# Kernel tuning notes

Hardware: AMD Instinct MI355X
Metric: run time of the kernel (lower is better)

The kernel has to match this reference:

```python
import jax, jax.numpy as jnp
import numpy as np

NUM_HEADS = 8


def setup_inputs() -> dict:
    key = jax.random.key(0)
    ks = jax.random.split(key, 16)
    B, Ct, Co, H, W = 1, 256, 128, 64, 64
    s = lambda k, *shape: jax.random.normal(k, shape, dtype=jnp.float32) * 0.02
    return {
        "thermal_features": jax.random.normal(ks[0], (B, Ct, H, W), dtype=jnp.float32),
        "optical_features": jax.random.normal(ks[1], (B, Co, H, W), dtype=jnp.float32),
        "emissivity_map": jax.random.uniform(ks[2], (B, 1, H, W), dtype=jnp.float32),
        "Wq": s(ks[3], Ct, Ct), "bq": jnp.zeros((Ct,), jnp.float32),
        "Wk": s(ks[4], Ct, Co), "bk": jnp.zeros((Ct,), jnp.float32),
        "Wv": s(ks[5], Ct, Co), "bv": jnp.zeros((Ct,), jnp.float32),
        "conv1_w": s(ks[6], 32, 1, 3, 3), "conv1_b": jnp.zeros((32,), jnp.float32),
        "conv2_w": s(ks[7], NUM_HEADS, 32, 1, 1), "conv2_b": jnp.zeros((NUM_HEADS,), jnp.float32),
        "Wp": s(ks[8], Ct, Ct), "bp": jnp.zeros((Ct,), jnp.float32),
    }


def reference(thermal_features, optical_features, emissivity_map,
              Wq, bq, Wk, bk, Wv, bv, conv1_w, conv1_b, conv2_w, conv2_b, Wp, bp):
    B, Ct, H, W = thermal_features.shape
    Co = optical_features.shape[1]
    N = H * W
    h = NUM_HEADS
    d = Ct // h
    scale = d ** (-0.5)

    # flatten spatial -> tokens: [B, N, C]
    t_flat = thermal_features.reshape(B, Ct, N).transpose(0, 2, 1)
    o_flat = optical_features.reshape(B, Co, N).transpose(0, 2, 1)

    # projections, split heads: [B, h, N, d]
    q = (t_flat @ Wq.T + bq).reshape(B, N, h, d).transpose(0, 2, 1, 3)
    k = (o_flat @ Wk.T + bk).reshape(B, N, h, d).transpose(0, 2, 1, 3)
    v = (o_flat @ Wv.T + bv).reshape(B, N, h, d).transpose(0, 2, 1, 3)

    # full attention scores: [B, h, N, N]
    attn = jnp.einsum('bhqd,bhkd->bhqk', q, k) * scale

    # emissivity gate: Conv(1->32, 3x3, pad 1) -> ReLU -> Conv(32->h, 1x1) -> Sigmoid
    g = jax.lax.conv_general_dilated(emissivity_map, conv1_w, (1, 1), 'SAME',
                                     dimension_numbers=('NCHW', 'OIHW', 'NCHW'))
    g = jax.nn.relu(g + conv1_b[None, :, None, None])
    g = jax.lax.conv_general_dilated(g, conv2_w, (1, 1), 'SAME',
                                     dimension_numbers=('NCHW', 'OIHW', 'NCHW'))
    g = jax.nn.sigmoid(g + conv2_b[None, :, None, None])  # [B, h, H, W]
    g = g.reshape(B, h, N)[..., None]  # [B, h, N, 1] gates query rows

    attn = jax.nn.softmax(attn * g, axis=-1)  # dropout is identity in eval

    out = jnp.einsum('bhqk,bhkd->bhqd', attn, v)  # [B, h, N, d]
    out = out.transpose(0, 2, 1, 3).reshape(B, N, Ct)
    out = out @ Wp.T + bp
    return out.transpose(0, 2, 1).reshape(B, Ct, H, W)
```

## Files before the change

kernel.cpp:

```cpp
#include <hip/hip_runtime.h>
#include <hip/hip_bf16.h>

#define N_TOK 4096
#define CT 256

typedef __attribute__((ext_vector_type(8))) short bf16x8;
typedef __attribute__((ext_vector_type(16))) float f32x16;

__device__ __forceinline__ unsigned pkbf(float a, float b) {
  float2 t; t.x = a; t.y = b;
  __hip_bfloat162 h = __float22bfloat162_rn(t);
  return *reinterpret_cast<unsigned*>(&h);
}

#if __has_builtin(__builtin_amdgcn_exp2f)
__device__ __forceinline__ float fexp2(float x) { return __builtin_amdgcn_exp2f(x); }
#else
__device__ __forceinline__ float fexp2(float x) { return exp2f(x); }
#endif

__global__ __launch_bounds__(256) void prep_kernel(
    const float* __restrict__ thermal, const float* __restrict__ optical,
    const float* __restrict__ Wq, const float* __restrict__ Wk,
    const float* __restrict__ Wv, const float* __restrict__ Wp,
    const float* __restrict__ em, const float* __restrict__ w1,
    const float* __restrict__ b1, const float* __restrict__ w2,
    const float* __restrict__ b2,
    unsigned short* __restrict__ Xbt, unsigned short* __restrict__ Xbo,
    unsigned short* __restrict__ Wall, float* __restrict__ g)
{
  __shared__ unsigned short tile[64][264];
  const int bx = blockIdx.x, tid = threadIdx.x;
  if (bx < 128) {
    const bool th = (bx < 64);
    const float* X = th ? thermal : optical;
    unsigned short* Xb = th ? Xbt : Xbo;
    const int CIN = th ? 256 : 128;
    const int n0 = (th ? bx : bx - 64) * 64;
    const int nl = tid & 63;
    const int cw = (tid >> 6) * 4;
    for (int c0 = 0; c0 < CIN; c0 += 16) {
      int c = c0 + cw;
      float x0 = X[(size_t)(c + 0) * N_TOK + n0 + nl];
      float x1 = X[(size_t)(c + 1) * N_TOK + n0 + nl];
      float x2 = X[(size_t)(c + 2) * N_TOK + n0 + nl];
      float x3 = X[(size_t)(c + 3) * N_TOK + n0 + nl];
      uint2 w; w.x = pkbf(x0, x1); w.y = pkbf(x2, x3);
      *(uint2*)&tile[nl][c] = w;
    }
    __syncthreads();
    const int n = tid >> 2, q = tid & 3;
    const int cb = q * (CIN / 4);
    for (int j = 0; j < CIN / 4; j += 4)
      *(uint2*)(Xb + (size_t)(n0 + n) * CIN + cb + j) = *(const uint2*)&tile[n][cb + j];
  } else if (bx < 224) {
    int i = (bx - 128) * 2048 + tid * 8;
    const float* src; int off;
    if (i < 65536)       { src = Wq; off = 0; }
    else if (i < 98304)  { src = Wk; off = 65536; }
    else if (i < 131072) { src = Wv; off = 98304; }
    else                 { src = Wp; off = 131072; }
    float4 f0 = *(const float4*)(src + (i - off));
    float4 f1 = *(const float4*)(src + (i - off) + 4);
    uint4 o;
    o.x = pkbf(f0.x, f0.y); o.y = pkbf(f0.z, f0.w);
    o.z = pkbf(f1.x, f1.y); o.w = pkbf(f1.z, f1.w);
    *(uint4*)(Wall + i) = o;
  } else {
    int n = (bx - 224) * 256 + tid;
    int y = n >> 6, x = n & 63;
    float e[9];
#pragma unroll
    for (int dy = 0; dy < 3; dy++)
#pragma unroll
      for (int dx = 0; dx < 3; dx++) {
        int yy = y + dy - 1, xx = x + dx - 1;
        e[dy * 3 + dx] = (yy >= 0 && yy < 64 && xx >= 0 && xx < 64)
                             ? em[yy * 64 + xx] : 0.f;
      }
    float c1[32];
#pragma unroll
    for (int oc = 0; oc < 32; oc++) {
      float a = b1[oc];
#pragma unroll
      for (int t = 0; t < 9; t++) a = fmaf(e[t], w1[oc * 9 + t], a);
      c1[oc] = fmaxf(a, 0.f);
    }
#pragma unroll
    for (int hh = 0; hh < 8; hh++) {
      float a = b2[hh];
#pragma unroll
      for (int oc = 0; oc < 32; oc++) a = fmaf(c1[oc], w2[hh * 32 + oc], a);
      g[hh * N_TOK + n] = 1.f / (1.f + __expf(-a));
    }
  }
}

template <int CIN>
__device__ __forceinline__ void gemm_tile(
    const unsigned short* __restrict__ xp, const unsigned short* __restrict__ wp,
    f32x16& accE, f32x16& accO)
{
#pragma unroll
  for (int c = 0; c < CIN; c += 32) {
    bf16x8 a0 = *(const bf16x8*)(xp + c);
    bf16x8 b0 = *(const bf16x8*)(wp + c);
    bf16x8 a1 = *(const bf16x8*)(xp + c + 16);
    bf16x8 b1 = *(const bf16x8*)(wp + c + 16);
    accE = __builtin_amdgcn_mfma_f32_32x32x16_bf16(a0, b0, accE, 0, 0, 0);
    accO = __builtin_amdgcn_mfma_f32_32x32x16_bf16(a1, b1, accO, 0, 0, 0);
  }
}

__global__ __launch_bounds__(256) void qkv_kernel(
    const unsigned short* __restrict__ Xbt, const unsigned short* __restrict__ Xbo,
    const unsigned short* __restrict__ Wall,
    const float* __restrict__ bq, const float* __restrict__ bk,
    const float* __restrict__ bv, const float* __restrict__ g,
    unsigned short* __restrict__ Qh, unsigned short* __restrict__ Kh,
    unsigned short* __restrict__ Vf)
{
  __shared__ float ldsT[4][32][33];
  const int tid = threadIdx.x;
  const int wave = tid >> 6, lane = tid & 63;
  const int l31 = lane & 31, hi = lane >> 5;
  const int y = blockIdx.y;
  const int head = y & 7;
  const int n0 = blockIdx.x * 128 + wave * 32;

  f32x16 accE, accO;
#pragma unroll
  for (int i = 0; i < 16; i++) { accE[i] = 0.f; accO[i] = 0.f; }
  float bo;
  if (y < 8) {
    gemm_tile<256>(Xbt + (size_t)(n0 + l31) * 256 + hi * 8,
                   Wall + (size_t)(head * 32 + l31) * 256 + hi * 8, accE, accO);
    bo = bq[head * 32 + l31];
  } else if (y < 16) {
    gemm_tile<128>(Xbo + (size_t)(n0 + l31) * 128 + hi * 8,
                   Wall + 65536 + (size_t)(head * 32 + l31) * 128 + hi * 8, accE, accO);
    bo = bk[head * 32 + l31];
  } else {
    gemm_tile<128>(Xbo + (size_t)(n0 + l31) * 128 + hi * 8,
                   Wall + 98304 + (size_t)(head * 32 + l31) * 128 + hi * 8, accE, accO);
    bo = bv[head * 32 + l31];
  }
  float val[16];
#pragma unroll
  for (int r = 0; r < 16; r++) val[r] = accE[r] + accO[r] + bo;

  if (y < 8) {
    const float QSC = 0.17677669529663689f * 1.4426950408889634f;
#pragma unroll
    for (int r = 0; r < 16; r++) {
      int t = n0 + (r & 3) + 8 * (r >> 2) + 4 * hi;
      val[r] *= QSC * g[head * N_TOK + t];
    }
  }

#pragma unroll
  for (int r = 0; r < 16; r++)
    ldsT[wave][(r & 3) + 8 * (r >> 2) + 4 * hi][l31] = val[r];

  if (y < 16) {
    unsigned pk[8];
#pragma unroll
    for (int i = 0; i < 8; i++)
      pk[i] = pkbf(ldsT[wave][l31][16 * hi + 2 * i],
                   ldsT[wave][l31][16 * hi + 2 * i + 1]);
    unsigned short* dst = (y < 8 ? Qh : Kh) +
        ((size_t)head * N_TOK + n0 + l31) * 32 + 16 * hi;
    *(uint4*)dst = make_uint4(pk[0], pk[1], pk[2], pk[3]);
    *(uint4*)(dst + 8) = make_uint4(pk[4], pk[5], pk[6], pk[7]);
  } else {
    unsigned pk[8];
#pragma unroll
    for (int i = 0; i < 8; i++)
      pk[i] = pkbf(ldsT[wave][16 * hi + 2 * i][l31],
                   ldsT[wave][16 * hi + 2 * i + 1][l31]);
    unsigned short* dst = Vf +
        (((size_t)head * 256 + (n0 >> 4) + hi) * 32 + l31) * 16;
    *(uint4*)dst = make_uint4(pk[0], pk[1], pk[2], pk[3]);
    *(uint4*)(dst + 8) = make_uint4(pk[4], pk[5], pk[6], pk[7]);
  }
}

__global__ __launch_bounds__(256, 4) void attn_kernel(
    const unsigned short* __restrict__ Qh, const unsigned short* __restrict__ Kh,
    const unsigned short* __restrict__ Vf,
    unsigned short* __restrict__ Ob, float* __restrict__ ls, int kps)
{
  __shared__ float ldsT[4][32][33];
  const int tid = threadIdx.x;
  const int wave = tid >> 6, lane = tid & 63;
  const int l31 = lane & 31, hi = lane >> 5;
  const int hh = blockIdx.x >> 5;
  const int qb = blockIdx.x & 31;
  const int split = blockIdx.y;
  const int qrow0 = qb * 128 + wave * 32;
  const int kbase0 = split * kps;

  const unsigned short* qrow = Qh + ((size_t)hh * N_TOK + qrow0 + l31) * 32;
  const bf16x8 qf0 = *(const bf16x8*)(qrow + hi * 8);
  const bf16x8 qf1 = *(const bf16x8*)(qrow + 16 + hi * 8);

  const unsigned short* kb_base = Kh + (size_t)hh * (N_TOK * 32);
  const unsigned short* vf_base = Vf + (size_t)hh * (256 * 32 * 16);

  f32x16 acc, zero16;
#pragma unroll
  for (int i = 0; i < 16; i++) { acc[i] = 0.f; zero16[i] = 0.f; }
  float lsum = 0.f;

#define LK(kb, s) (*(const bf16x8*)(kb_base + (size_t)((kb) + l31) * 32 + (s) * 16 + hi * 8))
#define LV(kt2)   (*(const bf16x8*)(vf_base + (size_t)((kt2) * 32 + l31) * 16 + hi * 8))

  bf16x8 kf0 = LK(kbase0, 0), kf1 = LK(kbase0, 1);
  bf16x8 vb0 = LV(kbase0 >> 4), vb1 = LV((kbase0 >> 4) + 1);

#pragma unroll 2
  for (int kt = 0; kt < kps; kt += 32) {
    const int nxt = (kt + 32 < kps) ? (kbase0 + kt + 32) : kbase0;
    bf16x8 nk0 = LK(nxt, 0), nk1 = LK(nxt, 1);
    bf16x8 nv0 = LV(nxt >> 4), nv1 = LV((nxt >> 4) + 1);

    f32x16 s = __builtin_amdgcn_mfma_f32_32x32x16_bf16(kf0, qf0, zero16, 0, 0, 0);
    s = __builtin_amdgcn_mfma_f32_32x32x16_bf16(kf1, qf1, s, 0, 0, 0);

    float p[16];
#pragma unroll
    for (int r = 0; r < 16; r++) p[r] = fexp2(s[r]);

    lsum += (((p[0] + p[1]) + (p[2] + p[3])) + ((p[4] + p[5]) + (p[6] + p[7]))) +
            (((p[8] + p[9]) + (p[10] + p[11])) + ((p[12] + p[13]) + (p[14] + p[15])));

    unsigned a0 = pkbf(p[0], p[1]),   a1 = pkbf(p[2], p[3]);
    unsigned b0 = pkbf(p[4], p[5]),   b1 = pkbf(p[6], p[7]);
    unsigned c0 = pkbf(p[8], p[9]),   c1 = pkbf(p[10], p[11]);
    unsigned d0 = pkbf(p[12], p[13]), d1 = pkbf(p[14], p[15]);
    asm("v_permlane32_swap_b32 %0, %1" : "+v"(a0), "+v"(b0));
    asm("v_permlane32_swap_b32 %0, %1" : "+v"(a1), "+v"(b1));
    asm("v_permlane32_swap_b32 %0, %1" : "+v"(c0), "+v"(d0));
    asm("v_permlane32_swap_b32 %0, %1" : "+v"(c1), "+v"(d1));
    union { unsigned w[4]; bf16x8 v; } u0, u1;
    u0.w[0] = a0; u0.w[1] = a1; u0.w[2] = b0; u0.w[3] = b1;
    u1.w[0] = c0; u1.w[1] = c1; u1.w[2] = d0; u1.w[3] = d1;

    acc = __builtin_amdgcn_mfma_f32_32x32x16_bf16(u0.v, vb0, acc, 0, 0, 0);
    acc = __builtin_amdgcn_mfma_f32_32x32x16_bf16(u1.v, vb1, acc, 0, 0, 0);

    kf0 = nk0; kf1 = nk1; vb0 = nv0; vb1 = nv1;
  }
#undef LK
#undef LV

  float lt = lsum + __shfl_xor(lsum, 32);
  if (hi == 0)
    ls[((size_t)split * 8 + hh) * N_TOK + qrow0 + l31] = lt;

#pragma unroll
  for (int r = 0; r < 16; r++)
    ldsT[wave][(r & 3) + 8 * (r >> 2) + 4 * hi][l31] = acc[r];
  unsigned pk[8];
#pragma unroll
  for (int i = 0; i < 8; i++)
    pk[i] = pkbf(ldsT[wave][l31][16 * hi + 2 * i],
                 ldsT[wave][l31][16 * hi + 2 * i + 1]);
  unsigned short* dst =
      Ob + (((size_t)split * 8 + hh) * N_TOK + qrow0 + l31) * 32 + 16 * hi;
  *(uint4*)dst = make_uint4(pk[0], pk[1], pk[2], pk[3]);
  *(uint4*)(dst + 8) = make_uint4(pk[4], pk[5], pk[6], pk[7]);
}

__global__ __launch_bounds__(256) void reduce_kernel(
    const unsigned short* __restrict__ Ob, const float* __restrict__ ls,
    unsigned short* __restrict__ Ab, int ksplit)
{
  int gid = blockIdx.x * 256 + threadIdx.x;
  int n = gid >> 5, c8 = (gid & 31) * 8;
  int hh = c8 >> 5, cc = c8 & 31;
  float o[8];
#pragma unroll
  for (int i = 0; i < 8; i++) o[i] = 0.f;
  float l = 0.f;
  for (int s = 0; s < ksplit; s++) {
    uint4 raw = *(const uint4*)(Ob + (((size_t)s * 8 + hh) * N_TOK + n) * 32 + cc);
    unsigned w[4] = {raw.x, raw.y, raw.z, raw.w};
#pragma unroll
    for (int i = 0; i < 4; i++) {
      o[2 * i]     += __uint_as_float(w[i] << 16);
      o[2 * i + 1] += __uint_as_float(w[i] & 0xffff0000u);
    }
    l += ls[((size_t)s * 8 + hh) * N_TOK + n];
  }
  float inv = 1.f / l;
  unsigned pk[4];
#pragma unroll
  for (int i = 0; i < 4; i++)
    pk[i] = pkbf(o[2 * i] * inv, o[2 * i + 1] * inv);
  *(uint4*)(Ab + (size_t)n * CT + c8) = make_uint4(pk[0], pk[1], pk[2], pk[3]);
}

__global__ __launch_bounds__(256) void pout_kernel(
    const unsigned short* __restrict__ Ab, const unsigned short* __restrict__ Wall,
    const float* __restrict__ bp, float* __restrict__ out)
{
  const int tid = threadIdx.x;
  const int wave = tid >> 6, lane = tid & 63;
  const int l31 = lane & 31, hi = lane >> 5;
  const int n0 = blockIdx.x * 128 + wave * 32;
  const int o0 = blockIdx.y * 32;

  f32x16 accE, accO;
#pragma unroll
  for (int i = 0; i < 16; i++) { accE[i] = 0.f; accO[i] = 0.f; }
  gemm_tile<256>(Ab + (size_t)(n0 + l31) * 256 + hi * 8,
                 Wall + 131072 + (size_t)(o0 + l31) * 256 + hi * 8, accE, accO);
  const float bo = bp[o0 + l31];
#pragma unroll
  for (int rr = 0; rr < 4; rr++) {
    float4 w = make_float4(accE[4 * rr + 0] + accO[4 * rr + 0] + bo,
                           accE[4 * rr + 1] + accO[4 * rr + 1] + bo,
                           accE[4 * rr + 2] + accO[4 * rr + 2] + bo,
                           accE[4 * rr + 3] + accO[4 * rr + 3] + bo);
    *(float4*)(out + (size_t)(o0 + l31) * N_TOK + n0 + 8 * rr + 4 * hi) = w;
  }
}

extern "C" void kernel_launch(void* const* d_in, const int* in_sizes, int n_in,
                              void* d_out, int out_size, void* d_ws, size_t ws_size,
                              hipStream_t stream)
{
  const float* thermal = (const float*)d_in[0];
  const float* optical = (const float*)d_in[1];
  const float* em      = (const float*)d_in[2];
  const float* Wq = (const float*)d_in[3];
  const float* bq = (const float*)d_in[4];
  const float* Wk = (const float*)d_in[5];
  const float* bk = (const float*)d_in[6];
  const float* Wv = (const float*)d_in[7];
  const float* bv = (const float*)d_in[8];
  const float* w1 = (const float*)d_in[9];
  const float* b1 = (const float*)d_in[10];
  const float* w2 = (const float*)d_in[11];
  const float* b2 = (const float*)d_in[12];
  const float* Wp = (const float*)d_in[13];
  const float* bp = (const float*)d_in[14];

  char* ws = (char*)d_ws;
  const size_t MB = 1u << 20;
  unsigned short* Xbt = (unsigned short*)(ws);
  unsigned short* Xbo = (unsigned short*)(ws + 2 * MB);
  unsigned short* Wall = (unsigned short*)(ws + 3 * MB);
  float* gbuf = (float*)(ws + 3 * MB + 512 * 1024);
  unsigned short* Qh = (unsigned short*)(ws + 4 * MB);
  unsigned short* Kh = (unsigned short*)(ws + 6 * MB);
  unsigned short* Vf = (unsigned short*)(ws + 8 * MB);
  unsigned short* Ab = (unsigned short*)(ws + 10 * MB);
  float* lsp = (float*)(ws + 12 * MB);
  unsigned short* Ob = (unsigned short*)(ws + 13 * MB);

  const int ksplit = (ws_size >= 29 * MB) ? 8 : 4;

  prep_kernel<<<240, 256, 0, stream>>>(thermal, optical, Wq, Wk, Wv, Wp,
                                       em, w1, b1, w2, b2, Xbt, Xbo, Wall, gbuf);
  qkv_kernel<<<dim3(32, 24), 256, 0, stream>>>(Xbt, Xbo, Wall, bq, bk, bv, gbuf,
                                               Qh, Kh, Vf);
  attn_kernel<<<dim3(256, ksplit), 256, 0, stream>>>(Qh, Kh, Vf, Ob, lsp,
                                                     N_TOK / ksplit);
  reduce_kernel<<<512, 256, 0, stream>>>(Ob, lsp, Ab, ksplit);
  pout_kernel<<<dim3(32, 8), 256, 0, stream>>>(Ab, Wall, bp, (float*)d_out);
}
```

Before: 70.42 us.

## Fuse split-K reduction into output projection and fix split count at four

Merges the split-K reduce kernel and the output projection GEMM into one kernel. The normalized attention output for a 32-token tile now stays in shared memory instead of going through a global buffer, and each wave computes two 32-channel output tiles from it. The attention split factor is also fixed at 4 instead of 8 when workspace allows, which halves reduction traffic but lowers attention-kernel parallelism. The fused kernel launches only 128 blocks, which may underfill the GPU.

Measured after the change: 78.42 us. 11.3% more time.

```diff
diff --git a/kernel.cpp b/kernel.cpp
--- a/kernel.cpp
+++ b/kernel.cpp
@@ -3,6 +3,7 @@
 
 #define N_TOK 4096
 #define CT 256
+#define KSPLIT 4
 
 typedef __attribute__((ext_vector_type(8))) short bf16x8;
 typedef __attribute__((ext_vector_type(16))) float f32x16;
@@ -272,58 +273,74 @@
   *(uint4*)(dst + 8) = make_uint4(pk[4], pk[5], pk[6], pk[7]);
 }
 
-__global__ __launch_bounds__(256) void reduce_kernel(
+__global__ __launch_bounds__(256) void redout_kernel(
     const unsigned short* __restrict__ Ob, const float* __restrict__ ls,
-    unsigned short* __restrict__ Ab, int ksplit)
-{
-  int gid = blockIdx.x * 256 + threadIdx.x;
-  int n = gid >> 5, c8 = (gid & 31) * 8;
-  int hh = c8 >> 5, cc = c8 & 31;
-  float o[8];
-#pragma unroll
-  for (int i = 0; i < 8; i++) o[i] = 0.f;
-  float l = 0.f;
-  for (int s = 0; s < ksplit; s++) {
-    uint4 raw = *(const uint4*)(Ob + (((size_t)s * 8 + hh) * N_TOK + n) * 32 + cc);
-    unsigned w[4] = {raw.x, raw.y, raw.z, raw.w};
-#pragma unroll
-    for (int i = 0; i < 4; i++) {
-      o[2 * i]     += __uint_as_float(w[i] << 16);
-      o[2 * i + 1] += __uint_as_float(w[i] & 0xffff0000u);
-    }
-    l += ls[((size_t)s * 8 + hh) * N_TOK + n];
-  }
-  float inv = 1.f / l;
-  unsigned pk[4];
-#pragma unroll
-  for (int i = 0; i < 4; i++)
-    pk[i] = pkbf(o[2 * i] * inv, o[2 * i + 1] * inv);
-  *(uint4*)(Ab + (size_t)n * CT + c8) = make_uint4(pk[0], pk[1], pk[2], pk[3]);
-}
-
-__global__ __launch_bounds__(256) void pout_kernel(
-    const unsigned short* __restrict__ Ab, const unsigned short* __restrict__ Wall,
-    const float* __restrict__ bp, float* __restrict__ out)
-{
+    const unsigned short* __restrict__ Wall, const float* __restrict__ bp,
+    float* __restrict__ out)
+{
+  __shared__ __align__(16) unsigned short A[32][264];
   const int tid = threadIdx.x;
+  const int n0 = blockIdx.x * 32;
+
+#pragma unroll
+  for (int rep = 0; rep < 4; rep++) {
+    int idx = rep * 256 + tid;
+    int nl = idx >> 5;
+    int c8 = (idx & 31) * 8;
+    int hh = c8 >> 5, cc = c8 & 31;
+    int n = n0 + nl;
+    float o[8];
+#pragma unroll
+    for (int i = 0; i < 8; i++) o[i] = 0.f;
+    float l = 0.f;
+#pragma unroll
+    for (int s = 0; s < KSPLIT; s++) {
+      uint4 raw = *(const uint4*)(Ob + (((size_t)s * 8 + hh) * N_TOK + n) * 32 + cc);
+      unsigned w[4] = {raw.x, raw.y, raw.z, raw.w};
+#pragma unroll
+      for (int i = 0; i < 4; i++) {
+        o[2 * i]     += __uint_as_float(w[i] << 16);
+        o[2 * i + 1] += __uint_as_float(w[i] & 0xffff0000u);
+      }
+      l += ls[((size_t)s * 8 + hh) * N_TOK + n];
+    }
+    float inv = 1.f / l;
+    uint4 pk;
+    pk.x = pkbf(o[0] * inv, o[1] * inv);
+    pk.y = pkbf(o[2] * inv, o[3] * inv);
+    pk.z = pkbf(o[4] * inv, o[5] * inv);
+    pk.w = pkbf(o[6] * inv, o[7] * inv);
+    *(uint4*)&A[nl][c8] = pk;
+  }
+  __syncthreads();
+
   const int wave = tid >> 6, lane = tid & 63;
   const int l31 = lane & 31, hi = lane >> 5;
-  const int n0 = blockIdx.x * 128 + wave * 32;
-  const int o0 = blockIdx.y * 32;
-
-  f32x16 accE, accO;
-#pragma unroll
-  for (int i = 0; i < 16; i++) { accE[i] = 0.f; accO[i] = 0.f; }
-  gemm_tile<256>(Ab + (size_t)(n0 + l31) * 256 + hi * 8,
-                 Wall + 131072 + (size_t)(o0 + l31) * 256 + hi * 8, accE, accO);
-  const float bo = bp[o0 + l31];
-#pragma unroll
-  for (int rr = 0; rr < 4; rr++) {
-    float4 w = make_float4(accE[4 * rr + 0] + accO[4 * rr + 0] + bo,
-                           accE[4 * rr + 1] + accO[4 * rr + 1] + bo,
-                           accE[4 * rr + 2] + accO[4 * rr + 2] + bo,
-                           accE[4 * rr + 3] + accO[4 * rr + 3] + bo);
-    *(float4*)(out + (size_t)(o0 + l31) * N_TOK + n0 + 8 * rr + 4 * hi) = w;
+#pragma unroll
+  for (int t = 0; t < 2; t++) {
+    const int o0 = (wave + 4 * t) * 32;
+    f32x16 accE, accO;
+#pragma unroll
+    for (int i = 0; i < 16; i++) { accE[i] = 0.f; accO[i] = 0.f; }
+    const unsigned short* wp = Wall + 131072 + (size_t)(o0 + l31) * 256 + hi * 8;
+#pragma unroll
+    for (int c = 0; c < 256; c += 32) {
+      bf16x8 a0 = *(const bf16x8*)&A[l31][c + hi * 8];
+      bf16x8 a1 = *(const bf16x8*)&A[l31][c + 16 + hi * 8];
+      bf16x8 b0 = *(const bf16x8*)(wp + c);
+      bf16x8 b1 = *(const bf16x8*)(wp + c + 16);
+      accE = __builtin_amdgcn_mfma_f32_32x32x16_bf16(a0, b0, accE, 0, 0, 0);
+      accO = __builtin_amdgcn_mfma_f32_32x32x16_bf16(a1, b1, accO, 0, 0, 0);
+    }
+    const float bo = bp[o0 + l31];
+#pragma unroll
+    for (int rr = 0; rr < 4; rr++) {
+      float4 w = make_float4(accE[4 * rr + 0] + accO[4 * rr + 0] + bo,
+                             accE[4 * rr + 1] + accO[4 * rr + 1] + bo,
+                             accE[4 * rr + 2] + accO[4 * rr + 2] + bo,
+                             accE[4 * rr + 3] + accO[4 * rr + 3] + bo);
+      *(float4*)(out + (size_t)(o0 + l31) * N_TOK + n0 + 8 * rr + 4 * hi) = w;
+    }
   }
 }
 
@@ -356,18 +373,14 @@
   unsigned short* Qh = (unsigned short*)(ws + 4 * MB);
   unsigned short* Kh = (unsigned short*)(ws + 6 * MB);
   unsigned short* Vf = (unsigned short*)(ws + 8 * MB);
-  unsigned short* Ab = (unsigned short*)(ws + 10 * MB);
   float* lsp = (float*)(ws + 12 * MB);
   unsigned short* Ob = (unsigned short*)(ws + 13 * MB);
-
-  const int ksplit = (ws_size >= 29 * MB) ? 8 : 4;
 
   prep_kernel<<<240, 256, 0, stream>>>(thermal, optical, Wq, Wk, Wv, Wp,
                                        em, w1, b1, w2, b2, Xbt, Xbo, Wall, gbuf);
   qkv_kernel<<<dim3(32, 24), 256, 0, stream>>>(Xbt, Xbo, Wall, bq, bk, bv, gbuf,
                                                Qh, Kh, Vf);
-  attn_kernel<<<dim3(256, ksplit), 256, 0, stream>>>(Qh, Kh, Vf, Ob, lsp,
-                                                     N_TOK / ksplit);
-  reduce_kernel<<<512, 256, 0, stream>>>(Ob, lsp, Ab, ksplit);
-  pout_kernel<<<dim3(32, 8), 256, 0, stream>>>(Ab, Wall, bp, (float*)d_out);
-}
+  attn_kernel<<<dim3(256, KSPLIT), 256, 0, stream>>>(Qh, Kh, Vf, Ob, lsp,
+                                                     N_TOK / KSPLIT);
+  redout_kernel<<<128, 256, 0, stream>>>(Ob, lsp, Wall, bp, (float*)d_out);
+}
```

## Split keys across waves within a block and combine partials in LDS

Applied to the files above, without the earlier changes.

The attention kernel now gives each block 32 query rows of one head, with its four waves each covering a quarter of the keys. Partial outputs and row sums are merged in shared memory after a block barrier. This removes the separate reduce kernel, the global round trip of bf16 partial outputs and sums, and one launch. In exchange the four waves of a block no longer share query rows, and the combine adds a synchronisation plus LDS traffic. Partials are also summed in fp32 rather than rounded to bf16 first.

Result: faster. 67.69 us (-3.9%).

```diff
diff --git a/kernel.cpp b/kernel.cpp
--- a/kernel.cpp
+++ b/kernel.cpp
@@ -157,7 +157,6 @@
       val[r] *= QSC * g[head * N_TOK + t];
     }
   }
-
 #pragma unroll
   for (int r = 0; r < 16; r++)
     ldsT[wave][(r & 3) + 8 * (r >> 2) + 4 * hi][l31] = val[r];
@@ -187,18 +186,17 @@
 
 __global__ __launch_bounds__(256, 4) void attn_kernel(
     const unsigned short* __restrict__ Qh, const unsigned short* __restrict__ Kh,
-    const unsigned short* __restrict__ Vf,
-    unsigned short* __restrict__ Ob, float* __restrict__ ls, int kps)
-{
-  __shared__ float ldsT[4][32][33];
+    const unsigned short* __restrict__ Vf, unsigned short* __restrict__ Ab)
+{
+  __shared__ float combA[4][32][33];
+  __shared__ float combL[4][32];
   const int tid = threadIdx.x;
   const int wave = tid >> 6, lane = tid & 63;
   const int l31 = lane & 31, hi = lane >> 5;
-  const int hh = blockIdx.x >> 5;
-  const int qb = blockIdx.x & 31;
-  const int split = blockIdx.y;
-  const int qrow0 = qb * 128 + wave * 32;
-  const int kbase0 = split * kps;
+  const int hh = blockIdx.x >> 7;
+  const int qb = blockIdx.x & 127;
+  const int qrow0 = qb * 32;
+  const int kbase0 = wave * 1024;
 
   const unsigned short* qrow = Qh + ((size_t)hh * N_TOK + qrow0 + l31) * 32;
   const bf16x8 qf0 = *(const bf16x8*)(qrow + hi * 8);
@@ -219,8 +217,8 @@
   bf16x8 vb0 = LV(kbase0 >> 4), vb1 = LV((kbase0 >> 4) + 1);
 
 #pragma unroll 2
-  for (int kt = 0; kt < kps; kt += 32) {
-    const int nxt = (kt + 32 < kps) ? (kbase0 + kt + 32) : kbase0;
+  for (int kt = 0; kt < 1024; kt += 32) {
+    const int nxt = (kt + 32 < 1024) ? (kbase0 + kt + 32) : kbase0;
     bf16x8 nk0 = LK(nxt, 0), nk1 = LK(nxt, 1);
     bf16x8 nv0 = LV(nxt >> 4), nv1 = LV((nxt >> 4) + 1);
 
@@ -255,50 +253,26 @@
 #undef LV
 
   float lt = lsum + __shfl_xor(lsum, 32);
-  if (hi == 0)
-    ls[((size_t)split * 8 + hh) * N_TOK + qrow0 + l31] = lt;
+  if (hi == 0) combL[wave][l31] = lt;
 
 #pragma unroll
   for (int r = 0; r < 16; r++)
-    ldsT[wave][(r & 3) + 8 * (r >> 2) + 4 * hi][l31] = acc[r];
-  unsigned pk[8];
-#pragma unroll
-  for (int i = 0; i < 8; i++)
-    pk[i] = pkbf(ldsT[wave][l31][16 * hi + 2 * i],
-                 ldsT[wave][l31][16 * hi + 2 * i + 1]);
-  unsigned short* dst =
-      Ob + (((size_t)split * 8 + hh) * N_TOK + qrow0 + l31) * 32 + 16 * hi;
-  *(uint4*)dst = make_uint4(pk[0], pk[1], pk[2], pk[3]);
-  *(uint4*)(dst + 8) = make_uint4(pk[4], pk[5], pk[6], pk[7]);
-}
-
-__global__ __launch_bounds__(256) void reduce_kernel(
-    const unsigned short* __restrict__ Ob, const float* __restrict__ ls,
-    unsigned short* __restrict__ Ab, int ksplit)
-{
-  int gid = blockIdx.x * 256 + threadIdx.x;
-  int n = gid >> 5, c8 = (gid & 31) * 8;
-  int hh = c8 >> 5, cc = c8 & 31;
-  float o[8];
-#pragma unroll
-  for (int i = 0; i < 8; i++) o[i] = 0.f;
-  float l = 0.f;
-  for (int s = 0; s < ksplit; s++) {
-    uint4 raw = *(const uint4*)(Ob + (((size_t)s * 8 + hh) * N_TOK + n) * 32 + cc);
-    unsigned w[4] = {raw.x, raw.y, raw.z, raw.w};
-#pragma unroll
-    for (int i = 0; i < 4; i++) {
-      o[2 * i]     += __uint_as_float(w[i] << 16);
-      o[2 * i + 1] += __uint_as_float(w[i] & 0xffff0000u);
-    }
-    l += ls[((size_t)s * 8 + hh) * N_TOK + n];
-  }
+    combA[wave][(r & 3) + 8 * (r >> 2) + 4 * hi][l31] = acc[r];
+  __syncthreads();
+
+  const int t = tid >> 3;
+  const int c4 = (tid & 7) * 4;
+  float l = combL[0][t] + combL[1][t] + combL[2][t] + combL[3][t];
   float inv = 1.f / l;
-  unsigned pk[4];
-#pragma unroll
-  for (int i = 0; i < 4; i++)
-    pk[i] = pkbf(o[2 * i] * inv, o[2 * i + 1] * inv);
-  *(uint4*)(Ab + (size_t)n * CT + c8) = make_uint4(pk[0], pk[1], pk[2], pk[3]);
+  float o[4];
+#pragma unroll
+  for (int j = 0; j < 4; j++)
+    o[j] = combA[0][t][c4 + j] + combA[1][t][c4 + j] +
+           combA[2][t][c4 + j] + combA[3][t][c4 + j];
+  uint2 pk;
+  pk.x = pkbf(o[0] * inv, o[1] * inv);
+  pk.y = pkbf(o[2] * inv, o[3] * inv);
+  *(uint2*)(Ab + (size_t)(qrow0 + t) * CT + hh * 32 + c4) = pk;
 }
 
 __global__ __launch_bounds__(256) void pout_kernel(
@@ -357,17 +331,11 @@
   unsigned short* Kh = (unsigned short*)(ws + 6 * MB);
   unsigned short* Vf = (unsigned short*)(ws + 8 * MB);
   unsigned short* Ab = (unsigned short*)(ws + 10 * MB);
-  float* lsp = (float*)(ws + 12 * MB);
-  unsigned short* Ob = (unsigned short*)(ws + 13 * MB);
-
-  const int ksplit = (ws_size >= 29 * MB) ? 8 : 4;
 
   prep_kernel<<<240, 256, 0, stream>>>(thermal, optical, Wq, Wk, Wv, Wp,
                                        em, w1, b1, w2, b2, Xbt, Xbo, Wall, gbuf);
   qkv_kernel<<<dim3(32, 24), 256, 0, stream>>>(Xbt, Xbo, Wall, bq, bk, bv, gbuf,
                                                Qh, Kh, Vf);
-  attn_kernel<<<dim3(256, ksplit), 256, 0, stream>>>(Qh, Kh, Vf, Ob, lsp,
-                                                     N_TOK / ksplit);
-  reduce_kernel<<<512, 256, 0, stream>>>(Ob, lsp, Ab, ksplit);
+  attn_kernel<<<1024, 256, 0, stream>>>(Qh, Kh, Vf, Ab);
   pout_kernel<<<dim3(32, 8), 256, 0, stream>>>(Ab, Wall, bp, (float*)d_out);
 }
```
